# Optimization experiments

Measured on AMD Instinct MI355X. Metric: run time of the kernel, lower is better.

The kernel has to match this reference:

```python
import jax, jax.numpy as jnp
import numpy as np

IN_C = 256
OUT_C = 256
KQ_C = 256
HEADS = 8

def setup_inputs() -> dict:
    key = jax.random.key(0)
    kx, kq, kk, kv = jax.random.split(key, 4)
    N, T = 4, 2048
    x = jax.random.normal(kx, (N, IN_C, T), dtype=jnp.float32)
    # Conv1d(kernel_size=1, bias=False) weights: [out, in]
    s = 1.0 / np.sqrt(IN_C)
    Wq = jax.random.uniform(kq, (KQ_C, IN_C), dtype=jnp.float32, minval=-s, maxval=s)
    Wk = jax.random.uniform(kk, (KQ_C, IN_C), dtype=jnp.float32, minval=-s, maxval=s)
    Wv = jax.random.uniform(kv, (OUT_C, IN_C), dtype=jnp.float32, minval=-s, maxval=s)
    return {"x": x, "Wq": Wq, "Wk": Wk, "Wv": Wv}

def reference(x, Wq, Wk, Wv):
    N, C, T = x.shape
    H = HEADS
    dk = KQ_C // H   # head dim for q/k
    dv = OUT_C // H  # head dim for v
    # 1x1 conv == channel matmul: [N,C,T] -> [N,out,T]
    q = jnp.einsum('oc,nct->not', Wq, x).reshape(N, H, dk, T)
    k = jnp.einsum('oc,nct->not', Wk, x).reshape(N, H, dk, T)
    v = jnp.einsum('oc,nct->not', Wv, x).reshape(N, H, dv, T)
    # scores: [N,H,T,T] = q^T k, scaled
    scores = jnp.einsum('nhdt,nhds->nhts', q, k) / np.sqrt(dk).astype(jnp.float32)
    attn = jax.nn.softmax(scores, axis=-1)
    # out: [N,H,T,dv] -> [N,H,dv,T] -> [N,OUT_C,T]
    out = jnp.einsum('nhts,nhds->nhdt', attn, v)
    return out.reshape(N, OUT_C, T)
```

## Files before the change

kernel.cpp:

```cpp
#include <hip/hip_runtime.h>


typedef float f32x4 __attribute__((ext_vector_type(4)));
typedef short short8 __attribute__((ext_vector_type(8)));
typedef short short4v __attribute__((ext_vector_type(4)));

#define WS_Q 0u
#define WS_K (4u << 20)
#define WS_V (8u << 20)
#define WS_X (12u << 20)
#define WS_W (16u << 20)
#define WS_OP (20u << 20)

__device__ __forceinline__ unsigned short f2bf(float f) {
  unsigned int u = __builtin_bit_cast(unsigned int, f);
  u += 0x7FFFu + ((u >> 16) & 1u);
  return (unsigned short)(u >> 16);
}

__device__ __forceinline__ int pack_bf16rn(float a, float b) {
  unsigned int ua = __builtin_bit_cast(unsigned int, a) + 0x8000u;
  unsigned int ub = __builtin_bit_cast(unsigned int, b) + 0x8000u;
  return __builtin_amdgcn_perm(ub, ua, 0x07060302);
}

__global__ __launch_bounds__(256) void pack_kernel(
    const float* __restrict__ x, const float* __restrict__ Wq,
    const float* __restrict__ Wk, const float* __restrict__ Wv,
    unsigned short* __restrict__ ws) {
  const int tid = threadIdx.x;
  const int lane = tid & 63;
  const int wv = tid >> 6;
  const int lc = lane & 15, lq = lane >> 4;
  const int b = blockIdx.x;
  alignas(16) unsigned short tmp[8];
  if (b < 1024) {
    const int r = b * 4 + wv;
    const int kc = r & 7, tt = (r >> 3) & 127, n = r >> 10;
    const int t = tt * 16 + lc;
    const int c0 = kc * 32 + lq * 8;
    const float* src = x + (size_t)(n * 256 + c0) * 2048 + t;
#pragma unroll
    for (int j = 0; j < 8; ++j) tmp[j] = f2bf(src[(size_t)j * 2048]);
    unsigned short* dst = ws + (WS_X >> 1) + (size_t)r * 512 + lane * 8;
    *(int4*)dst = *(const int4*)tmp;
  } else {
    const int r = (b - 1024) * 4 + wv;
    const int kc = r & 7, ot = (r >> 3) & 15, wi = r >> 7;
    const float* W = (wi == 0) ? Wq : (wi == 1) ? Wk : Wv;
    const float scale = (wi == 0) ? 0.25503492f : 1.0f;
    const int o = ot * 16 + lc;
    const int c0 = kc * 32 + lq * 8;
    const float* src = W + o * 256 + c0;
#pragma unroll
    for (int j = 0; j < 8; ++j) tmp[j] = f2bf(src[j] * scale);
    unsigned short* dst = ws + (WS_W >> 1) + (size_t)r * 512 + lane * 8;
    *(int4*)dst = *(const int4*)tmp;
  }
}

__global__ __launch_bounds__(256) void proj_kernel(unsigned short* __restrict__ ws) {
  __shared__ unsigned short eps[4][2048];
  const int tid = threadIdx.x, lane = tid & 63, w = tid >> 6;
  const int lc = lane & 15, lq = lane >> 4;
  const int tt2 = blockIdx.x;
  const int n = blockIdx.y;
  const int wi = blockIdx.z;
  const unsigned short* Xb = ws + (WS_X >> 1);
  const unsigned short* Wb = ws + (WS_W >> 1);

  short8 af[2][8];
#pragma unroll
  for (int mt = 0; mt < 2; ++mt)
#pragma unroll
    for (int kc = 0; kc < 8; ++kc)
      af[mt][kc] = *(const short8*)(Xb + ((size_t)((n * 128 + tt2 * 2 + mt) * 8 + kc) * 512 + lane * 8));

  f32x4 acc[2][4];
#pragma unroll
  for (int mt = 0; mt < 2; ++mt)
#pragma unroll
    for (int nt = 0; nt < 4; ++nt) {
      f32x4 z = {0.f, 0.f, 0.f, 0.f};
      acc[mt][nt] = z;
    }

#pragma unroll
  for (int kc = 0; kc < 8; ++kc) {
    short8 bf[4];
#pragma unroll
    for (int nt = 0; nt < 4; ++nt)
      bf[nt] = *(const short8*)(Wb + ((size_t)((wi * 16 + w * 4 + nt) * 8 + kc) * 512 + lane * 8));
#pragma unroll
    for (int mt = 0; mt < 2; ++mt)
#pragma unroll
      for (int nt = 0; nt < 4; ++nt)
        acc[mt][nt] = __builtin_amdgcn_mfma_f32_16x16x32_bf16(af[mt][kc], bf[nt], acc[mt][nt], 0, 0, 0);
  }

  if (wi < 2) {
    unsigned short* ep = eps[w];
#pragma unroll
    for (int mt = 0; mt < 2; ++mt)
#pragma unroll
      for (int nt = 0; nt < 4; ++nt) {
        const int m2 = ((nt & 1) << 1) | (lc >> 3);
        const int base = ((mt * 2 + (nt >> 1)) << 9) + (m2 << 7) + (lq << 5) + (lc & 7);
#pragma unroll
        for (int r = 0; r < 4; ++r)
          ep[base + ((r ^ m2) << 3)] = f2bf(acc[mt][nt][r]);
      }
    const int swzl = lane ^ (lane >> 4);
    unsigned short* dst = ws + ((wi == 0) ? (WS_Q >> 1) : (WS_K >> 1));
#pragma unroll
    for (int rl = 0; rl < 4; ++rl) {
      int4 v = *(const int4*)(ep + (rl << 9) + swzl * 8);
      const int mt = rl >> 1, hh = rl & 1;
      const int nh = n * 8 + w * 2 + hh;
      const int ttg = tt2 * 2 + mt;
      *(int4*)(dst + ((size_t)(nh * 128 + ttg) * 64 + lane) * 8) = v;
    }
  } else {
    const int kb = tt2 >> 1, sbp = tt2 & 1;
#pragma unroll
    for (int nt = 0; nt < 4; ++nt) {
      const int nh = n * 8 + w * 2 + (nt >> 1);
      const int dt = nt & 1;
      alignas(16) unsigned short tmp[8];
#pragma unroll
      for (int mt = 0; mt < 2; ++mt)
#pragma unroll
        for (int r = 0; r < 4; ++r) tmp[mt * 4 + r] = f2bf(acc[mt][nt][r]);
      unsigned short* dstv = ws + (WS_V >> 1) +
          ((size_t)((((nh * 32 + kb) * 2 + dt) * 2 + sbp)) * 64 + lane) * 8;
      *(int4*)dstv = *(const int4*)tmp;
    }
  }
}

template <int KS>
__global__ __launch_bounds__(128, 5) void attn_kernel(
    const unsigned short* __restrict__ ws, float* __restrict__ out,
    unsigned short* __restrict__ opart, float* __restrict__ lpart) {
  const int tid = threadIdx.x;
  const int lane = tid & 63, wv = tid >> 6;
  const int lc = lane & 15, quad = lane >> 4;
  constexpr int CH = 32 * KS;
  const int c = blockIdx.x & (CH - 1);
  const int qx = blockIdx.x / CH;
  const int nh = c & 31;
  const int ks = c >> 5;
  const int qw = qx * 2 + wv;
  constexpr int NKB = 32 / KS;
  const int kb0 = ks * NKB;

  const unsigned short* Qw = ws + (WS_Q >> 1) + ((size_t)(nh * 128 + qw * 2)) * 512;
  const unsigned short* Kb = ws + (WS_K >> 1) + (size_t)nh * 65536;
  const unsigned short* Vb = ws + (WS_V >> 1) + (size_t)nh * 65536;

  short8 qf[2];
  qf[0] = *(const short8*)(Qw + lane * 8);
  qf[1] = *(const short8*)(Qw + 512 + lane * 8);

  f32x4 acc[2][2];
#pragma unroll
  for (int mt = 0; mt < 2; ++mt)
#pragma unroll
    for (int dt = 0; dt < 2; ++dt) {
      f32x4 z = {0.f, 0.f, 0.f, 0.f};
      acc[mt][dt] = z;
    }
  float lsum[2] = {0.f, 0.f};

  for (int kb = kb0; kb < kb0 + NKB; ++kb) {
    const unsigned short* kp = Kb + (size_t)kb * 2048 + lane * 8;
    const unsigned short* vp = Vb + (size_t)kb * 2048 + lane * 8;
    short8 kf[4], vvr[4];
#pragma unroll
    for (int sb = 0; sb < 4; ++sb) kf[sb] = *(const short8*)(kp + sb * 512);
#pragma unroll
    for (int u = 0; u < 4; ++u) vvr[u] = *(const short8*)(vp + u * 512);

    short4v pf[2][4];
#pragma unroll
    for (int mt = 0; mt < 2; ++mt) {
      f32x4 st[4];
#pragma unroll
      for (int sb = 0; sb < 4; ++sb) {
        f32x4 z = {0.f, 0.f, 0.f, 0.f};
        st[sb] = __builtin_amdgcn_mfma_f32_16x16x32_bf16(kf[sb], qf[mt], z, 0, 0, 0);
      }
#pragma unroll
      for (int sb = 0; sb < 4; ++sb) {
        float p0 = __builtin_amdgcn_exp2f(st[sb][0]);
        float p1 = __builtin_amdgcn_exp2f(st[sb][1]);
        float p2 = __builtin_amdgcn_exp2f(st[sb][2]);
        float p3 = __builtin_amdgcn_exp2f(st[sb][3]);
        lsum[mt] += (p0 + p1) + (p2 + p3);
        int2 pi;
        pi.x = pack_bf16rn(p0, p1);
        pi.y = pack_bf16rn(p2, p3);
        pf[mt][sb] = __builtin_bit_cast(short4v, pi);
      }
    }

    short4v vf[4][2];
#pragma unroll
    for (int dt = 0; dt < 2; ++dt)
#pragma unroll
      for (int sbp = 0; sbp < 2; ++sbp) {
        short8 t = vvr[dt * 2 + sbp];
        vf[sbp * 2 + 0][dt] = __builtin_shufflevector(t, t, 0, 1, 2, 3);
        vf[sbp * 2 + 1][dt] = __builtin_shufflevector(t, t, 4, 5, 6, 7);
      }
#pragma unroll
    for (int sb = 0; sb < 4; ++sb)
#pragma unroll
      for (int mt = 0; mt < 2; ++mt) {
        acc[mt][0] = __builtin_amdgcn_mfma_f32_16x16x16bf16_1k(pf[mt][sb], vf[sb][0], acc[mt][0], 0, 0, 0);
        acc[mt][1] = __builtin_amdgcn_mfma_f32_16x16x16bf16_1k(pf[mt][sb], vf[sb][1], acc[mt][1], 0, 0, 0);
      }
  }

#pragma unroll
  for (int mt = 0; mt < 2; ++mt) {
    lsum[mt] += __shfl_xor(lsum[mt], 16);
    lsum[mt] += __shfl_xor(lsum[mt], 32);
  }

  if constexpr (KS == 1) {
    const int chbase = (nh >> 3) * 256 + (nh & 7) * 32;
#pragma unroll
    for (int mt = 0; mt < 2; ++mt) {
      float is[4];
#pragma unroll
      for (int r = 0; r < 4; ++r) is[r] = 1.0f / __shfl(lsum[mt], quad * 4 + r);
      const int tb = qw * 32 + mt * 16 + quad * 4;
#pragma unroll
      for (int dt = 0; dt < 2; ++dt) {
        f32x4 ov;
#pragma unroll
        for (int r = 0; r < 4; ++r) ov[r] = acc[mt][dt][r] * is[r];
        *(f32x4*)(out + (size_t)(chbase + dt * 16 + lc) * 2048 + tb) = ov;
      }
    }
  } else {
    const size_t ob = (size_t)(ks * 32 + nh) * 32 * 2048;
#pragma unroll
    for (int mt = 0; mt < 2; ++mt) {
      const int tb = qw * 32 + mt * 16 + quad * 4;
#pragma unroll
      for (int dt = 0; dt < 2; ++dt) {
        int2 pi;
        pi.x = pack_bf16rn(acc[mt][dt][0], acc[mt][dt][1]);
        pi.y = pack_bf16rn(acc[mt][dt][2], acc[mt][dt][3]);
        *(int2*)(opart + ob + (size_t)(dt * 16 + lc) * 2048 + tb) = pi;
      }
      if (quad == 0)
        lpart[(size_t)(ks * 32 + nh) * 2048 + qw * 32 + mt * 16 + lc] = lsum[mt];
    }
  }
}

template <int KS>
__global__ __launch_bounds__(256) void finalize_kernel(
    const unsigned short* __restrict__ opart, const float* __restrict__ lpart,
    float* __restrict__ out) {
  const int f = blockIdx.x * 256 + threadIdx.x;
  const int t4 = f & 511;
  const int c = f >> 9;
  const int n = c >> 8, ch = c & 255;
  const int nh = n * 8 + (ch >> 5), d = ch & 31;
  float o[4] = {0.f, 0.f, 0.f, 0.f};
  float l[4] = {0.f, 0.f, 0.f, 0.f};
#pragma unroll
  for (int ks = 0; ks < KS; ++ks) {
    const short4v ov = *(const short4v*)(opart + ((size_t)(ks * 32 + nh) * 32 + d) * 2048 + t4 * 4);
    const float4 lv = *(const float4*)(lpart + (size_t)(ks * 32 + nh) * 2048 + t4 * 4);
#pragma unroll
    for (int i = 0; i < 4; ++i) {
      const unsigned int u = ((unsigned int)(unsigned short)ov[i]) << 16;
      o[i] += __builtin_bit_cast(float, u);
    }
    l[0] += lv.x; l[1] += lv.y; l[2] += lv.z; l[3] += lv.w;
  }
  float4 r;
  r.x = o[0] / l[0]; r.y = o[1] / l[1]; r.z = o[2] / l[2]; r.w = o[3] / l[3];
  *(float4*)(out + (size_t)f * 4) = r;
}

extern "C" void kernel_launch(void* const* d_in, const int* in_sizes, int n_in,
                              void* d_out, int out_size, void* d_ws, size_t ws_size,
                              hipStream_t stream) {
  const float* x = (const float*)d_in[0];
  const float* Wq = (const float*)d_in[1];
  const float* Wk = (const float*)d_in[2];
  const float* Wv = (const float*)d_in[3];
  unsigned short* ws = (unsigned short*)d_ws;
  float* out = (float*)d_out;
  (void)in_sizes; (void)n_in; (void)out_size;

  pack_kernel<<<1120, 256, 0, stream>>>(x, Wq, Wk, Wv, ws);
  proj_kernel<<<dim3(64, 4, 3), 256, 0, stream>>>(ws);

  char* wsb = (char*)d_ws;
  unsigned short* opart = (unsigned short*)(wsb + WS_OP);
  if (ws_size >= ((size_t)41u << 20)) {
    float* lpart = (float*)(wsb + WS_OP + ((size_t)4 * 4u << 20));
    attn_kernel<4><<<4096, 128, 0, stream>>>(ws, out, opart, lpart);
    finalize_kernel<4><<<2048, 256, 0, stream>>>(opart, lpart, out);
  } else if (ws_size >= ((size_t)30u << 20)) {
    float* lpart = (float*)(wsb + WS_OP + ((size_t)2 * 4u << 20));
    attn_kernel<2><<<2048, 128, 0, stream>>>(ws, out, opart, lpart);
    finalize_kernel<2><<<2048, 256, 0, stream>>>(opart, lpart, out);
  } else {
    attn_kernel<1><<<1024, 128, 0, stream>>>(ws, out, nullptr, nullptr);
  }
}
```

Measured before the change: 111.0 us.

## Software-pipeline K/V loads in attention loop and drop 4-way key split

After: 107.8 us. 1.03x faster.

```diff
diff --git a/kernel.cpp b/kernel.cpp
--- a/kernel.cpp
+++ b/kernel.cpp
@@ -139,7 +139,7 @@
 }
 
 template <int KS>
-__global__ __launch_bounds__(128, 5) void attn_kernel(
+__global__ __launch_bounds__(128, 4) void attn_kernel(
     const unsigned short* __restrict__ ws, float* __restrict__ out,
     unsigned short* __restrict__ opart, float* __restrict__ lpart) {
   const int tid = threadIdx.x;
@@ -172,44 +172,43 @@
     }
   float lsum[2] = {0.f, 0.f};
 
-  for (int kb = kb0; kb < kb0 + NKB; ++kb) {
+  auto load_k = [&](short8 kf[4], int kb) {
     const unsigned short* kp = Kb + (size_t)kb * 2048 + lane * 8;
+#pragma unroll
+    for (int sb = 0; sb < 4; ++sb) kf[sb] = *(const short8*)(kp + sb * 512);
+  };
+  auto load_v = [&](short8 vv[4], int kb) {
     const unsigned short* vp = Vb + (size_t)kb * 2048 + lane * 8;
-    short8 kf[4], vvr[4];
-#pragma unroll
-    for (int sb = 0; sb < 4; ++sb) kf[sb] = *(const short8*)(kp + sb * 512);
-#pragma unroll
-    for (int u = 0; u < 4; ++u) vvr[u] = *(const short8*)(vp + u * 512);
-
-    short4v pf[2][4];
-#pragma unroll
-    for (int mt = 0; mt < 2; ++mt) {
-      f32x4 st[4];
+#pragma unroll
+    for (int u = 0; u < 4; ++u) vv[u] = *(const short8*)(vp + u * 512);
+  };
+
+  auto do_qk = [&](const short8 kf[4], short4v pf[2][4]) {
+#pragma unroll
+    for (int mt = 0; mt < 2; ++mt)
 #pragma unroll
       for (int sb = 0; sb < 4; ++sb) {
         f32x4 z = {0.f, 0.f, 0.f, 0.f};
-        st[sb] = __builtin_amdgcn_mfma_f32_16x16x32_bf16(kf[sb], qf[mt], z, 0, 0, 0);
-      }
-#pragma unroll
-      for (int sb = 0; sb < 4; ++sb) {
-        float p0 = __builtin_amdgcn_exp2f(st[sb][0]);
-        float p1 = __builtin_amdgcn_exp2f(st[sb][1]);
-        float p2 = __builtin_amdgcn_exp2f(st[sb][2]);
-        float p3 = __builtin_amdgcn_exp2f(st[sb][3]);
+        f32x4 st = __builtin_amdgcn_mfma_f32_16x16x32_bf16(kf[sb], qf[mt], z, 0, 0, 0);
+        float p0 = __builtin_amdgcn_exp2f(st[0]);
+        float p1 = __builtin_amdgcn_exp2f(st[1]);
+        float p2 = __builtin_amdgcn_exp2f(st[2]);
+        float p3 = __builtin_amdgcn_exp2f(st[3]);
         lsum[mt] += (p0 + p1) + (p2 + p3);
         int2 pi;
         pi.x = pack_bf16rn(p0, p1);
         pi.y = pack_bf16rn(p2, p3);
         pf[mt][sb] = __builtin_bit_cast(short4v, pi);
       }
-    }
-
+  };
+
+  auto do_pv = [&](const short8 vv[4], const short4v pf[2][4]) {
     short4v vf[4][2];
 #pragma unroll
     for (int dt = 0; dt < 2; ++dt)
 #pragma unroll
       for (int sbp = 0; sbp < 2; ++sbp) {
-        short8 t = vvr[dt * 2 + sbp];
+        short8 t = vv[dt * 2 + sbp];
         vf[sbp * 2 + 0][dt] = __builtin_shufflevector(t, t, 0, 1, 2, 3);
         vf[sbp * 2 + 1][dt] = __builtin_shufflevector(t, t, 4, 5, 6, 7);
       }
@@ -220,6 +219,33 @@
         acc[mt][0] = __builtin_amdgcn_mfma_f32_16x16x16bf16_1k(pf[mt][sb], vf[sb][0], acc[mt][0], 0, 0, 0);
         acc[mt][1] = __builtin_amdgcn_mfma_f32_16x16x16bf16_1k(pf[mt][sb], vf[sb][1], acc[mt][1], 0, 0, 0);
       }
+  };
+
+  short8 kf[4], vA[4], vB[4];
+  load_k(kf, kb0);
+  load_v(vA, kb0);
+  int kb = kb0;
+  for (; kb < kb0 + NKB - 2; kb += 2) {
+    short4v pfA[2][4];
+    do_qk(kf, pfA);
+    load_k(kf, kb + 1);
+    load_v(vB, kb + 1);
+    do_pv(vA, pfA);
+    short4v pfB[2][4];
+    do_qk(kf, pfB);
+    load_k(kf, kb + 2);
+    load_v(vA, kb + 2);
+    do_pv(vB, pfB);
+  }
+  {
+    short4v pfA[2][4];
+    do_qk(kf, pfA);
+    load_k(kf, kb + 1);
+    load_v(vB, kb + 1);
+    do_pv(vA, pfA);
+    short4v pfB[2][4];
+    do_qk(kf, pfB);
+    do_pv(vB, pfB);
   }
 
 #pragma unroll
@@ -305,11 +331,7 @@
 
   char* wsb = (char*)d_ws;
   unsigned short* opart = (unsigned short*)(wsb + WS_OP);
-  if (ws_size >= ((size_t)41u << 20)) {
-    float* lpart = (float*)(wsb + WS_OP + ((size_t)4 * 4u << 20));
-    attn_kernel<4><<<4096, 128, 0, stream>>>(ws, out, opart, lpart);
-    finalize_kernel<4><<<2048, 256, 0, stream>>>(opart, lpart, out);
-  } else if (ws_size >= ((size_t)30u << 20)) {
+  if (ws_size >= ((size_t)30u << 20)) {
     float* lpart = (float*)(wsb + WS_OP + ((size_t)2 * 4u << 20));
     attn_kernel<2><<<2048, 128, 0, stream>>>(ws, out, opart, lpart);
     finalize_kernel<2><<<2048, 256, 0, stream>>>(opart, lpart, out);
```

## Double query rows per wave, prefetch K/V, compute row sums via MFMA

Applied to the files above, without the earlier changes.

After: 113.0 us. No clear change (+1.8%).

```diff
diff --git a/kernel.cpp b/kernel.cpp
--- a/kernel.cpp
+++ b/kernel.cpp
@@ -139,7 +139,7 @@
 }
 
 template <int KS>
-__global__ __launch_bounds__(128, 5) void attn_kernel(
+__global__ __launch_bounds__(128, 3) void attn_kernel(
     const unsigned short* __restrict__ ws, float* __restrict__ out,
     unsigned short* __restrict__ opart, float* __restrict__ lpart) {
   const int tid = threadIdx.x;
@@ -154,88 +154,92 @@
   constexpr int NKB = 32 / KS;
   const int kb0 = ks * NKB;
 
-  const unsigned short* Qw = ws + (WS_Q >> 1) + ((size_t)(nh * 128 + qw * 2)) * 512;
+  const unsigned short* Qw = ws + (WS_Q >> 1) + ((size_t)(nh * 128 + qw * 4)) * 512;
   const unsigned short* Kb = ws + (WS_K >> 1) + (size_t)nh * 65536;
   const unsigned short* Vb = ws + (WS_V >> 1) + (size_t)nh * 65536;
 
-  short8 qf[2];
-  qf[0] = *(const short8*)(Qw + lane * 8);
-  qf[1] = *(const short8*)(Qw + 512 + lane * 8);
-
-  f32x4 acc[2][2];
-#pragma unroll
-  for (int mt = 0; mt < 2; ++mt)
-#pragma unroll
-    for (int dt = 0; dt < 2; ++dt) {
-      f32x4 z = {0.f, 0.f, 0.f, 0.f};
-      acc[mt][dt] = z;
-    }
-  float lsum[2] = {0.f, 0.f};
-
+  short8 qf[4];
+#pragma unroll
+  for (int mt = 0; mt < 4; ++mt)
+    qf[mt] = *(const short8*)(Qw + mt * 512 + lane * 8);
+
+  f32x4 acc[4][2];
+  f32x4 lsum_acc[4];
+#pragma unroll
+  for (int mt = 0; mt < 4; ++mt) {
+    f32x4 z = {0.f, 0.f, 0.f, 0.f};
+    acc[mt][0] = z;
+    acc[mt][1] = z;
+    lsum_acc[mt] = z;
+  }
+  const short4v onesf = {(short)0x3F80, (short)0x3F80, (short)0x3F80, (short)0x3F80};
+
+  short8 kf[4], vv[4];
+  {
+    const unsigned short* kp = Kb + (size_t)kb0 * 2048 + lane * 8;
+    const unsigned short* vp = Vb + (size_t)kb0 * 2048 + lane * 8;
+#pragma unroll
+    for (int u = 0; u < 4; ++u) kf[u] = *(const short8*)(kp + u * 512);
+#pragma unroll
+    for (int u = 0; u < 4; ++u) vv[u] = *(const short8*)(vp + u * 512);
+  }
+
+#pragma unroll 2
   for (int kb = kb0; kb < kb0 + NKB; ++kb) {
-    const unsigned short* kp = Kb + (size_t)kb * 2048 + lane * 8;
-    const unsigned short* vp = Vb + (size_t)kb * 2048 + lane * 8;
-    short8 kf[4], vvr[4];
-#pragma unroll
-    for (int sb = 0; sb < 4; ++sb) kf[sb] = *(const short8*)(kp + sb * 512);
-#pragma unroll
-    for (int u = 0; u < 4; ++u) vvr[u] = *(const short8*)(vp + u * 512);
-
-    short4v pf[2][4];
-#pragma unroll
-    for (int mt = 0; mt < 2; ++mt) {
+    const unsigned short* nkp = Kb + (size_t)(kb + 1) * 2048 + lane * 8;
+    const unsigned short* nvp = Vb + (size_t)(kb + 1) * 2048 + lane * 8;
+#pragma unroll
+    for (int sb = 0; sb < 4; ++sb) {
+      const short8 t0 = vv[(sb >> 1)];
+      const short8 t1 = vv[2 + (sb >> 1)];
+      short4v vf0, vf1;
+      if (sb & 1) {
+        vf0 = __builtin_shufflevector(t0, t0, 4, 5, 6, 7);
+        vf1 = __builtin_shufflevector(t1, t1, 4, 5, 6, 7);
+      } else {
+        vf0 = __builtin_shufflevector(t0, t0, 0, 1, 2, 3);
+        vf1 = __builtin_shufflevector(t1, t1, 0, 1, 2, 3);
+      }
       f32x4 st[4];
 #pragma unroll
-      for (int sb = 0; sb < 4; ++sb) {
+      for (int mt = 0; mt < 4; ++mt) {
         f32x4 z = {0.f, 0.f, 0.f, 0.f};
-        st[sb] = __builtin_amdgcn_mfma_f32_16x16x32_bf16(kf[sb], qf[mt], z, 0, 0, 0);
-      }
-#pragma unroll
-      for (int sb = 0; sb < 4; ++sb) {
-        float p0 = __builtin_amdgcn_exp2f(st[sb][0]);
-        float p1 = __builtin_amdgcn_exp2f(st[sb][1]);
-        float p2 = __builtin_amdgcn_exp2f(st[sb][2]);
-        float p3 = __builtin_amdgcn_exp2f(st[sb][3]);
-        lsum[mt] += (p0 + p1) + (p2 + p3);
+        st[mt] = __builtin_amdgcn_mfma_f32_16x16x32_bf16(kf[sb], qf[mt], z, 0, 0, 0);
+      }
+      kf[sb] = *(const short8*)(nkp + sb * 512);
+      if (sb == 1) {
+        vv[0] = *(const short8*)(nvp + 0 * 512);
+        vv[2] = *(const short8*)(nvp + 2 * 512);
+      }
+      if (sb == 3) {
+        vv[1] = *(const short8*)(nvp + 1 * 512);
+        vv[3] = *(const short8*)(nvp + 3 * 512);
+      }
+#pragma unroll
+      for (int mt = 0; mt < 4; ++mt) {
+        const float p0 = __builtin_amdgcn_exp2f(st[mt][0]);
+        const float p1 = __builtin_amdgcn_exp2f(st[mt][1]);
+        const float p2 = __builtin_amdgcn_exp2f(st[mt][2]);
+        const float p3 = __builtin_amdgcn_exp2f(st[mt][3]);
         int2 pi;
         pi.x = pack_bf16rn(p0, p1);
         pi.y = pack_bf16rn(p2, p3);
-        pf[mt][sb] = __builtin_bit_cast(short4v, pi);
-      }
-    }
-
-    short4v vf[4][2];
-#pragma unroll
-    for (int dt = 0; dt < 2; ++dt)
-#pragma unroll
-      for (int sbp = 0; sbp < 2; ++sbp) {
-        short8 t = vvr[dt * 2 + sbp];
-        vf[sbp * 2 + 0][dt] = __builtin_shufflevector(t, t, 0, 1, 2, 3);
-        vf[sbp * 2 + 1][dt] = __builtin_shufflevector(t, t, 4, 5, 6, 7);
-      }
-#pragma unroll
-    for (int sb = 0; sb < 4; ++sb)
-#pragma unroll
-      for (int mt = 0; mt < 2; ++mt) {
-        acc[mt][0] = __builtin_amdgcn_mfma_f32_16x16x16bf16_1k(pf[mt][sb], vf[sb][0], acc[mt][0], 0, 0, 0);
-        acc[mt][1] = __builtin_amdgcn_mfma_f32_16x16x16bf16_1k(pf[mt][sb], vf[sb][1], acc[mt][1], 0, 0, 0);
-      }
-  }
-
-#pragma unroll
-  for (int mt = 0; mt < 2; ++mt) {
-    lsum[mt] += __shfl_xor(lsum[mt], 16);
-    lsum[mt] += __shfl_xor(lsum[mt], 32);
+        const short4v pf = __builtin_bit_cast(short4v, pi);
+        lsum_acc[mt] = __builtin_amdgcn_mfma_f32_16x16x16bf16_1k(pf, onesf, lsum_acc[mt], 0, 0, 0);
+        acc[mt][0] = __builtin_amdgcn_mfma_f32_16x16x16bf16_1k(pf, vf0, acc[mt][0], 0, 0, 0);
+        acc[mt][1] = __builtin_amdgcn_mfma_f32_16x16x16bf16_1k(pf, vf1, acc[mt][1], 0, 0, 0);
+      }
+    }
   }
 
   if constexpr (KS == 1) {
     const int chbase = (nh >> 3) * 256 + (nh & 7) * 32;
 #pragma unroll
-    for (int mt = 0; mt < 2; ++mt) {
-      float is[4];
-#pragma unroll
-      for (int r = 0; r < 4; ++r) is[r] = 1.0f / __shfl(lsum[mt], quad * 4 + r);
-      const int tb = qw * 32 + mt * 16 + quad * 4;
+    for (int mt = 0; mt < 4; ++mt) {
+      f32x4 is;
+#pragma unroll
+      for (int r = 0; r < 4; ++r) is[r] = 1.0f / lsum_acc[mt][r];
+      const int tb = qw * 64 + mt * 16 + quad * 4;
 #pragma unroll
       for (int dt = 0; dt < 2; ++dt) {
         f32x4 ov;
@@ -247,8 +251,8 @@
   } else {
     const size_t ob = (size_t)(ks * 32 + nh) * 32 * 2048;
 #pragma unroll
-    for (int mt = 0; mt < 2; ++mt) {
-      const int tb = qw * 32 + mt * 16 + quad * 4;
+    for (int mt = 0; mt < 4; ++mt) {
+      const int tb = qw * 64 + mt * 16 + quad * 4;
 #pragma unroll
       for (int dt = 0; dt < 2; ++dt) {
         int2 pi;
@@ -256,8 +260,8 @@
         pi.y = pack_bf16rn(acc[mt][dt][2], acc[mt][dt][3]);
         *(int2*)(opart + ob + (size_t)(dt * 16 + lc) * 2048 + tb) = pi;
       }
-      if (quad == 0)
-        lpart[(size_t)(ks * 32 + nh) * 2048 + qw * 32 + mt * 16 + lc] = lsum[mt];
+      if (lc == 0)
+        *(f32x4*)(lpart + (size_t)(ks * 32 + nh) * 2048 + qw * 64 + mt * 16 + quad * 4) = lsum_acc[mt];
     }
   }
 }
@@ -307,13 +311,13 @@
   unsigned short* opart = (unsigned short*)(wsb + WS_OP);
   if (ws_size >= ((size_t)41u << 20)) {
     float* lpart = (float*)(wsb + WS_OP + ((size_t)4 * 4u << 20));
-    attn_kernel<4><<<4096, 128, 0, stream>>>(ws, out, opart, lpart);
+    attn_kernel<4><<<2048, 128, 0, stream>>>(ws, out, opart, lpart);
     finalize_kernel<4><<<2048, 256, 0, stream>>>(opart, lpart, out);
   } else if (ws_size >= ((size_t)30u << 20)) {
     float* lpart = (float*)(wsb + WS_OP + ((size_t)2 * 4u << 20));
-    attn_kernel<2><<<2048, 128, 0, stream>>>(ws, out, opart, lpart);
+    attn_kernel<2><<<1024, 128, 0, stream>>>(ws, out, opart, lpart);
     finalize_kernel<2><<<2048, 256, 0, stream>>>(opart, lpart, out);
   } else {
-    attn_kernel<1><<<1024, 128, 0, stream>>>(ws, out, nullptr, nullptr);
-  }
-}
+    attn_kernel<1><<<512, 128, 0, stream>>>(ws, out, nullptr, nullptr);
+  }
+}
```
